# Kernel tuning notes

Hardware: AMD Instinct MI355X
Metric: run time of the kernel (lower is better)

The kernel has to match this reference:

```python
import jax, jax.numpy as jnp
import numpy as np

D, H, K = 384, 6, 8

def _ln(x, g, b, eps=1e-5):
    mu = jnp.mean(x, axis=-1, keepdims=True)
    var = jnp.mean((x - mu) ** 2, axis=-1, keepdims=True)
    return (x - mu) * jax.lax.rsqrt(var + eps) * g + b

def setup_inputs() -> dict:
    key = jax.random.key(0)
    ks = jax.random.split(key, 20)
    B, N = 4, 2048
    s = 0.02
    inp = {
        'x': jax.random.normal(ks[0], (B, N, D), jnp.float32),
        'knn_index': jax.random.randint(ks[1], (B * K * N,), 0, B * N, jnp.int64),
        'ln1_g': jnp.ones((D,), jnp.float32),
        'ln1_b': jnp.zeros((D,), jnp.float32),
        'w_qkv': jax.random.normal(ks[2], (D, 3 * D), jnp.float32) * s,
        'w_proj': jax.random.normal(ks[3], (D, D), jnp.float32) * s,
        'b_proj': jnp.zeros((D,), jnp.float32),
        'w_knn': jax.random.normal(ks[4], (2 * D, D), jnp.float32) * s,
        'b_knn': jnp.zeros((D,), jnp.float32),
        'w_g1': jax.random.normal(ks[5], (2 * D, D), jnp.float32) * s,
        'b_g1': jnp.zeros((D,), jnp.float32),
        'w_g2': jax.random.normal(ks[6], (D, D), jnp.float32) * s,
        'b_g2': jnp.zeros((D,), jnp.float32),
        'ln2_g': jnp.ones((D,), jnp.float32),
        'ln2_b': jnp.zeros((D,), jnp.float32),
        'w_fc1': jax.random.normal(ks[7], (D, 4 * D), jnp.float32) * s,
        'b_fc1': jnp.zeros((4 * D,), jnp.float32),
        'w_fc2': jax.random.normal(ks[8], (4 * D, D), jnp.float32) * s,
        'b_fc2': jnp.zeros((D,), jnp.float32),
    }
    return inp

def reference(x, knn_index, ln1_g, ln1_b, w_qkv, w_proj, b_proj, w_knn, b_knn,
              w_g1, b_g1, w_g2, b_g2, ln2_g, ln2_b, w_fc1, b_fc1, w_fc2, b_fc2):
    B, N, _ = x.shape
    hd = D // H
    scale = hd ** -0.5
    nx = _ln(x, ln1_g, ln1_b)
    # --- self attention ---
    qkv = (nx @ w_qkv).reshape(B, N, 3, H, hd).transpose(2, 0, 3, 1, 4)  # [3,B,H,N,hd]
    q, k, v = qkv[0], qkv[1], qkv[2]
    attn = jax.nn.softmax(jnp.einsum('bhnd,bhmd->bhnm', q * scale, k), axis=-1)
    attn_out = jnp.einsum('bhnm,bhmd->bhnd', attn, v).transpose(0, 2, 1, 3).reshape(B, N, D)
    attn_out = attn_out @ w_proj + b_proj
    # --- EdgeConv-style graph feature: gather-concat-MLP-maxpool ---
    feat = nx.reshape(B * N, D)[knn_index].reshape(B, K, N, D)
    xe = jnp.broadcast_to(nx[:, None], (B, K, N, D))
    gf = jnp.concatenate([feat - xe, xe], axis=-1)  # [B,K,N,2D]
    knn_out = jnp.max(jax.nn.leaky_relu(gf @ w_knn + b_knn, 0.2), axis=1)  # [B,N,D]
    # --- salience gate ---
    gi = jnp.concatenate([attn_out, knn_out], axis=-1)
    gate = jax.nn.sigmoid(jax.nn.gelu(gi @ w_g1 + b_g1, approximate=False) @ w_g2 + b_g2)
    fused = (1 - gate) * attn_out + gate * knn_out
    x = x + fused
    # --- FFN ---
    h = jax.nn.gelu(_ln(x, ln2_g, ln2_b) @ w_fc1 + b_fc1, approximate=False)
    x = x + (h @ w_fc2 + b_fc2)
    return x
```

## Files before the change

kernel.cpp:

```cpp
#include <hip/hip_runtime.h>
#include <math.h>

typedef unsigned short u16;
typedef __attribute__((ext_vector_type(8))) short short8;
typedef __attribute__((ext_vector_type(4))) float floatx4;
typedef __attribute__((ext_vector_type(4))) short sh4v;

union sh4u { sh4v v; u16 u[4]; };
union sh8u { short8 v; u16 u[8]; };

__device__ __forceinline__ floatx4 mfma16(short8 a, short8 b, floatx4 c) {
  return __builtin_amdgcn_mfma_f32_16x16x32_bf16(a, b, c, 0, 0, 0);
}

__device__ __forceinline__ floatx4 zero4() {
  floatx4 z = {0.f, 0.f, 0.f, 0.f};
  return z;
}

__device__ __forceinline__ u16 f2b(float f) {
  union { float f; unsigned u; } v; v.f = f;
  unsigned u = v.u;
  return (u16)((u + 0x7FFFu + ((u >> 16) & 1u)) >> 16);
}

__device__ __forceinline__ float b2f(u16 u) {
  union { unsigned u; float f; } v; v.u = ((unsigned)u) << 16;
  return v.f;
}

__device__ __forceinline__ float gelu_exact(float x) {
  return 0.5f * x * (1.f + erff(x * 0.70710678118654752440f));
}

__device__ __forceinline__ unsigned pack2(float a, float b) {
  return (unsigned)f2b(a) | ((unsigned)f2b(b) << 16);
}

__device__ __forceinline__ unsigned permpack(float p0, float p1) {
  return __builtin_amdgcn_perm(__float_as_uint(p1), __float_as_uint(p0), 0x07060302u);
}

__global__ __launch_bounds__(256) void tcln_kernel(
    const float* __restrict__ p0, const float* __restrict__ p1,
    const float* __restrict__ p2, const float* __restrict__ p3,
    const float* __restrict__ p4, const float* __restrict__ p5,
    const float* __restrict__ wknn,
    u16* __restrict__ o0, u16* __restrict__ o1, u16* __restrict__ o2,
    u16* __restrict__ o3, u16* __restrict__ o4, u16* __restrict__ o5,
    u16* __restrict__ wcT,
    const float* __restrict__ x, const float* __restrict__ g,
    const float* __restrict__ bia, u16* __restrict__ nx) {
  __shared__ u16 L[64][66];
  int t = blockIdx.x, tid = threadIdx.x;
  if (t >= 612) {
    int wave = tid >> 6, lane = tid & 63;
    int row = (t - 612) * 4 + wave;
    const float* xr = x + (size_t)row * 384;
    float v[6];
    float s = 0.f;
#pragma unroll
    for (int j = 0; j < 6; j++) { v[j] = xr[lane + 64 * j]; s += v[j]; }
#pragma unroll
    for (int off = 32; off > 0; off >>= 1) s += __shfl_xor(s, off);
    float mu = s * (1.f / 384.f);
    float ss = 0.f;
#pragma unroll
    for (int j = 0; j < 6; j++) { float d = v[j] - mu; ss += d * d; }
#pragma unroll
    for (int off = 32; off > 0; off >>= 1) ss += __shfl_xor(ss, off);
    float rstd = rsqrtf(ss * (1.f / 384.f) + 1e-5f);
    u16* orow = nx + (size_t)row * 384;
#pragma unroll
    for (int j = 0; j < 6; j++) {
      int d = lane + 64 * j;
      orow[d] = f2b((v[j] - mu) * rstd * g[d] + bia[d]);
    }
    return;
  }
  if (t >= 540) {
    t -= 540;
    int tk = t / 12, tn = t % 12;
    int k0 = tk * 64, j0 = tn * 64;
#pragma unroll
    for (int i = 0; i < 4; i++) {
      int c = tid + 256 * i;
      int r = c >> 4, c4 = (c & 15) * 4;
      floatx4 v;
      if (j0 < 384) {
        v = *(const floatx4*)(wknn + (size_t)(k0 + r) * 384 + j0 + c4);
      } else {
        floatx4 a = *(const floatx4*)(wknn + (size_t)(384 + k0 + r) * 384 + (j0 - 384) + c4);
        floatx4 b = *(const floatx4*)(wknn + (size_t)(k0 + r) * 384 + (j0 - 384) + c4);
        v = a - b;
      }
      *(unsigned*)&L[r][c4]     = pack2(v[0], v[1]);
      *(unsigned*)&L[r][c4 + 2] = pack2(v[2], v[3]);
    }
    __syncthreads();
#pragma unroll
    for (int i = 0; i < 2; i++) {
      int c = tid + 256 * i;
      int nn = c >> 3, k8 = (c & 7) * 8;
      sh8u pk;
#pragma unroll
      for (int j = 0; j < 8; j++) pk.u[j] = L[k8 + j][nn];
      *(short8*)(wcT + (size_t)(j0 + nn) * 384 + k0 + k8) = pk.v;
    }
    return;
  }
  const float* src; u16* dst; int Kd, Nd, tk, tn;
  if      (t < 108) { src = p0; dst = o0; Kd = 384;  Nd = 1152; tk = t / 18; tn = t % 18; }
  else if (t < 144) { src = p1; dst = o1; Kd = 384;  Nd = 384;  t -= 108; tk = t / 6;  tn = t % 6; }
  else if (t < 216) { src = p2; dst = o2; Kd = 768;  Nd = 384;  t -= 144; tk = t / 6;  tn = t % 6; }
  else if (t < 252) { src = p3; dst = o3; Kd = 384;  Nd = 384;  t -= 216; tk = t / 6;  tn = t % 6; }
  else if (t < 396) { src = p4; dst = o4; Kd = 384;  Nd = 1536; t -= 252; tk = t / 24; tn = t % 24; }
  else              { src = p5; dst = o5; Kd = 1536; Nd = 384;  t -= 396; tk = t / 6;  tn = t % 6; }
  int k0 = tk * 64, n0 = tn * 64;
#pragma unroll
  for (int i = 0; i < 4; i++) {
    int c = tid + 256 * i;
    int r = c >> 4, c4 = (c & 15) * 4;
    floatx4 v = *(const floatx4*)(src + (size_t)(k0 + r) * Nd + n0 + c4);
    *(unsigned*)&L[r][c4]     = pack2(v[0], v[1]);
    *(unsigned*)&L[r][c4 + 2] = pack2(v[2], v[3]);
  }
  __syncthreads();
#pragma unroll
  for (int i = 0; i < 2; i++) {
    int c = tid + 256 * i;
    int nn = c >> 3, k8 = (c & 7) * 8;
    sh8u pk;
#pragma unroll
    for (int j = 0; j < 8; j++) pk.u[j] = L[k8 + j][nn];
    *(short8*)(dst + (size_t)(n0 + nn) * Kd + k0 + k8) = pk.v;
  }
}

__global__ __launch_bounds__(256) void lnb_kernel(const u16* __restrict__ x,
                                                  const float* __restrict__ g,
                                                  const float* __restrict__ bia,
                                                  u16* __restrict__ out) {
  int wave = threadIdx.x >> 6, lane = threadIdx.x & 63;
  int row = blockIdx.x * 4 + wave;
  const u16* xr = x + (size_t)row * 384;
  float v[6];
  float s = 0.f;
#pragma unroll
  for (int j = 0; j < 6; j++) { v[j] = b2f(xr[lane + 64 * j]); s += v[j]; }
#pragma unroll
  for (int off = 32; off > 0; off >>= 1) s += __shfl_xor(s, off);
  float mu = s * (1.f / 384.f);
  float ss = 0.f;
#pragma unroll
  for (int j = 0; j < 6; j++) { float d = v[j] - mu; ss += d * d; }
#pragma unroll
  for (int off = 32; off > 0; off >>= 1) ss += __shfl_xor(ss, off);
  float rstd = rsqrtf(ss * (1.f / 384.f) + 1e-5f);
  u16* orow = out + (size_t)row * 384;
#pragma unroll
  for (int j = 0; j < 6; j++) {
    int d = lane + 64 * j;
    orow[d] = f2b((v[j] - mu) * rstd * g[d] + bia[d]);
  }
}

template <int EPI>
__global__ __launch_bounds__(256) void gemm128_kernel(
    const u16* __restrict__ A0, const u16* __restrict__ BwT,
    const u16* __restrict__ BwT2, int N, int K,
    const float* __restrict__ bias, u16* __restrict__ outB, u16* __restrict__ outB2,
    u16* __restrict__ outV) {
  __shared__ u16 As[128][72];
  __shared__ u16 Bs[128][72];
  int tid = threadIdx.x;
  int lane = tid & 63, wave = tid >> 6, quad = lane >> 4, l16 = lane & 15;
  int n0 = blockIdx.x * 128, m0 = blockIdx.y * 128;
  int wm = (wave >> 1) * 64, wn = (wave & 1) * 64;
  const u16* Bsrc = BwT;
  int nbase = n0;
  if (EPI == 8 && n0 >= 1152) { Bsrc = BwT2; nbase = n0 - 1152; }
  floatx4 acc[4][4];
#pragma unroll
  for (int i = 0; i < 4; i++)
#pragma unroll
    for (int j = 0; j < 4; j++) acc[i][j] = zero4();

  for (int k0 = 0; k0 < K; k0 += 64) {
#pragma unroll
    for (int i = 0; i < 4; i++) {
      int c = tid + 256 * i;
      int row = c >> 3, c8 = (c & 7) * 8;
      *(short8*)&As[row][c8] =
          *(const short8*)(A0 + (size_t)(m0 + row) * K + k0 + c8);
      *(short8*)&Bs[row][c8] =
          *(const short8*)(Bsrc + (size_t)(nbase + row) * K + k0 + c8);
    }
    __syncthreads();
#pragma unroll
    for (int kh = 0; kh < 2; kh++) {
      short8 af[4], bfr[4];
#pragma unroll
      for (int ti = 0; ti < 4; ti++)
        af[ti] = *(const short8*)&As[wm + ti * 16 + l16][kh * 32 + quad * 8];
#pragma unroll
      for (int tj = 0; tj < 4; tj++)
        bfr[tj] = *(const short8*)&Bs[wn + tj * 16 + l16][kh * 32 + quad * 8];
#pragma unroll
      for (int ti = 0; ti < 4; ti++)
#pragma unroll
        for (int tj = 0; tj < 4; tj++)
          acc[ti][tj] = mfma16(af[ti], bfr[tj], acc[ti][tj]);
    }
    __syncthreads();
  }

#pragma unroll
  for (int ti = 0; ti < 4; ti++)
#pragma unroll
    for (int tj = 0; tj < 4; tj++) {
      int col = n0 + wn + tj * 16 + l16;
      int row0 = m0 + wm + ti * 16 + quad * 4;
      if (EPI == 8) {
        if (n0 < 1152) {
          float sc = (col < 384) ? 0.18033688011112042f : 1.f;
          sh4u pk;
#pragma unroll
          for (int r = 0; r < 4; r++) {
            u16 bv = f2b(acc[ti][tj][r] * sc);
            outB[(size_t)(row0 + r) * 1152 + col] = bv;
            pk.u[r] = bv;
          }
          if (col >= 768) {
            int b = row0 >> 11, n = row0 & 2047;
            int hd = col - 768;
            *(sh4v*)(outV + ((size_t)(b * 6 + (hd >> 6)) * 64 + (hd & 63)) * 2048 + n) = pk.v;
          }
        } else {
#pragma unroll
          for (int r = 0; r < 4; r++)
            outB2[(size_t)(row0 + r) * 768 + (col - 1152)] = f2b(acc[ti][tj][r]);
        }
      } else {
#pragma unroll
        for (int r = 0; r < 4; r++)
          outB[(size_t)(row0 + r) * N + col] = f2b(gelu_exact(acc[ti][tj][r] + bias[col]));
      }
    }
}

template <int EPI>
__global__ __launch_bounds__(256) void gemm64_kernel(
    const u16* __restrict__ A0, const u16* __restrict__ A1, int Ksplit,
    const u16* __restrict__ BwT, int N, int K,
    const float* __restrict__ bias,
    float* __restrict__ outF, u16* __restrict__ outB,
    const u16* __restrict__ eA16, const u16* __restrict__ eK16,
    const float* __restrict__ eX) {
  __shared__ u16 As[64][72];
  __shared__ u16 Bs[128][72];
  int tid = threadIdx.x;
  int lane = tid & 63, w = tid >> 6, quad = lane >> 4, l16 = lane & 15;
  int n0 = blockIdx.x * 128, m0 = blockIdx.y * 64;
  int ra = tid >> 3, ca = (tid & 7) * 8;
  floatx4 acc[4][2];
#pragma unroll
  for (int i = 0; i < 4; i++)
#pragma unroll
    for (int j = 0; j < 2; j++) acc[i][j] = zero4();

  short8 pa[2], pb[4];
  auto loadAB = [&](int k0) {
    const u16* Ap;
    int kk, sA;
    if (k0 < Ksplit) { Ap = A0; kk = k0; sA = Ksplit; }
    else             { Ap = A1; kk = k0 - Ksplit; sA = K - Ksplit; }
    pa[0] = *(const short8*)(Ap + (size_t)(m0 + ra) * sA + kk + ca);
    pa[1] = *(const short8*)(Ap + (size_t)(m0 + ra + 32) * sA + kk + ca);
#pragma unroll
    for (int i = 0; i < 4; i++)
      pb[i] = *(const short8*)(BwT + (size_t)(n0 + ra + 32 * i) * K + k0 + ca);
  };
  loadAB(0);
  int iters = K >> 6;
  for (int kt = 0; kt < iters; kt++) {
    __syncthreads();
    *(short8*)&As[ra][ca] = pa[0];
    *(short8*)&As[ra + 32][ca] = pa[1];
#pragma unroll
    for (int i = 0; i < 4; i++) *(short8*)&Bs[ra + 32 * i][ca] = pb[i];
    __syncthreads();
    if (kt + 1 < iters) loadAB((kt + 1) * 64);
#pragma unroll
    for (int kh = 0; kh < 2; kh++) {
      short8 af[4], bfr[2];
#pragma unroll
      for (int mt = 0; mt < 4; mt++)
        af[mt] = *(const short8*)&As[mt * 16 + l16][kh * 32 + quad * 8];
#pragma unroll
      for (int nt = 0; nt < 2; nt++)
        bfr[nt] = *(const short8*)&Bs[w * 32 + nt * 16 + l16][kh * 32 + quad * 8];
#pragma unroll
      for (int mt = 0; mt < 4; mt++)
#pragma unroll
        for (int nt = 0; nt < 2; nt++)
          acc[mt][nt] = mfma16(af[mt], bfr[nt], acc[mt][nt]);
    }
  }

#pragma unroll
  for (int mt = 0; mt < 4; mt++)
#pragma unroll
    for (int nt = 0; nt < 2; nt++) {
      int col = n0 + w * 32 + nt * 16 + l16;
      int row0 = m0 + mt * 16 + quad * 4;
#pragma unroll
      for (int r = 0; r < 4; r++) {
        size_t rc = (size_t)(row0 + r) * N + col;
        float v = acc[mt][nt][r];
        if (EPI == 3) {
          outB[rc] = f2b(gelu_exact(v + bias[col]));
        } else if (EPI == 4) {
          float gte = 1.f / (1.f + __expf(-(v + bias[col])));
          float fu = (1.f - gte) * b2f(eA16[rc]) + gte * b2f(eK16[rc]);
          outB[rc] = f2b(eX[rc] + fu);
        } else if (EPI == 7) {
          outF[rc] = v + bias[col] + b2f(eA16[rc]);
        }
      }
    }
}

__global__ __launch_bounds__(256) void attn1_kernel(const u16* __restrict__ qkv,
                                                    const u16* __restrict__ Vt,
                                                    u16* __restrict__ OPb,
                                                    float* __restrict__ LS) {
  __shared__ u16 Ks[64][72];
  __shared__ u16 Vts[64][72];
  __shared__ u16 Ps[4][32][72];
  int tid = threadIdx.x;
  int lane = tid & 63, w = tid >> 6, quad = lane >> 4, l16 = lane & 15;
  int bh = blockIdx.y, b = bh / 6, h = bh % 6;
  int q0 = blockIdx.x * 128, split = blockIdx.z;
  const u16* qbase = qkv + (size_t)b * 2048 * 1152 + h * 64;
  const u16* kbase = qbase + 384 + (size_t)split * 512 * 1152;
  const u16* vtb = Vt + (size_t)bh * 64 * 2048 + split * 512;
  short8 qf[2][2];
#pragma unroll
  for (int s = 0; s < 2; s++) {
    int qrow = q0 + w * 32 + s * 16 + l16;
    qf[s][0] = *(const short8*)(qbase + (size_t)qrow * 1152 + quad * 8);
    qf[s][1] = *(const short8*)(qbase + (size_t)qrow * 1152 + 32 + quad * 8);
  }
  short8 ones;
#pragma unroll
  for (int j = 0; j < 8; j++) ones[j] = (short)0x3F80;
  floatx4 O[4][2];
  floatx4 accL[2] = {zero4(), zero4()};
#pragma unroll
  for (int i = 0; i < 4; i++)
#pragma unroll
    for (int s = 0; s < 2; s++) O[i][s] = zero4();

  int rb = tid >> 3, c8 = (tid & 7) * 8;
  short8 rk[2], rv[2];
  rk[0] = *(const short8*)(kbase + (size_t)rb * 1152 + c8);
  rk[1] = *(const short8*)(kbase + (size_t)(rb + 32) * 1152 + c8);
  rv[0] = *(const short8*)(vtb + (size_t)rb * 2048 + c8);
  rv[1] = *(const short8*)(vtb + (size_t)(rb + 32) * 2048 + c8);

  for (int kt = 0; kt < 8; kt++) {
    __syncthreads();
    *(short8*)&Ks[rb][c8] = rk[0];
    *(short8*)&Ks[rb + 32][c8] = rk[1];
    *(short8*)&Vts[rb][c8] = rv[0];
    *(short8*)&Vts[rb + 32][c8] = rv[1];
    __syncthreads();
    if (kt < 7) {
      int key0 = (kt + 1) * 64;
      rk[0] = *(const short8*)(kbase + (size_t)(key0 + rb) * 1152 + c8);
      rk[1] = *(const short8*)(kbase + (size_t)(key0 + rb + 32) * 1152 + c8);
      rv[0] = *(const short8*)(vtb + (size_t)rb * 2048 + key0 + c8);
      rv[1] = *(const short8*)(vtb + (size_t)(rb + 32) * 2048 + key0 + c8);
    }
#pragma unroll
    for (int mt = 0; mt < 4; mt++) {
      short8 k0 = *(const short8*)&Ks[mt * 16 + l16][quad * 8];
      short8 k1 = *(const short8*)&Ks[mt * 16 + l16][32 + quad * 8];
#pragma unroll
      for (int s = 0; s < 2; s++) {
        floatx4 st = mfma16(k0, qf[s][0], zero4());
        st = mfma16(k1, qf[s][1], st);
        uint2 pk;
        pk.x = permpack(exp2f(st[0]), exp2f(st[1]));
        pk.y = permpack(exp2f(st[2]), exp2f(st[3]));
        *(uint2*)&Ps[w][s * 16 + l16][mt * 16 + quad * 4] = pk;
      }
    }
    short8 pf[2][2];
#pragma unroll
    for (int s = 0; s < 2; s++) {
      pf[s][0] = *(const short8*)&Ps[w][s * 16 + l16][quad * 8];
      pf[s][1] = *(const short8*)&Ps[w][s * 16 + l16][32 + quad * 8];
      accL[s] = mfma16(ones, pf[s][0], accL[s]);
      accL[s] = mfma16(ones, pf[s][1], accL[s]);
    }
#pragma unroll
    for (int mt2 = 0; mt2 < 4; mt2++) {
      short8 v0 = *(const short8*)&Vts[mt2 * 16 + l16][quad * 8];
      short8 v1 = *(const short8*)&Vts[mt2 * 16 + l16][32 + quad * 8];
#pragma unroll
      for (int s = 0; s < 2; s++) {
        O[mt2][s] = mfma16(v0, pf[s][0], O[mt2][s]);
        O[mt2][s] = mfma16(v1, pf[s][1], O[mt2][s]);
      }
    }
  }
#pragma unroll
  for (int s = 0; s < 2; s++) {
    int row = b * 2048 + q0 + w * 32 + s * 16 + l16;
    u16* orow = OPb + (size_t)split * 8192 * 384 + (size_t)row * 384 + h * 64;
#pragma unroll
    for (int mt2 = 0; mt2 < 4; mt2++) {
      sh4u pk;
#pragma unroll
      for (int r = 0; r < 4; r++) pk.u[r] = f2b(O[mt2][s][r]);
      *(sh4v*)(orow + mt2 * 16 + quad * 4) = pk.v;
    }
    if (quad == 0) LS[split * 8192 + row] = accL[s][0];
  }
}

__global__ __launch_bounds__(256) void projknn_kernel(
    const u16* __restrict__ OPb, const float* __restrict__ LS,
    const u16* __restrict__ BwT, const float* __restrict__ bias,
    u16* __restrict__ outB,
    const u16* __restrict__ GBb, const int* __restrict__ kidx,
    const float* __restrict__ bknn, u16* __restrict__ knn_bf) {
  __shared__ u16 As[128][72];
  __shared__ u16 Bs[128][72];
  int bid = blockIdx.x, tid = threadIdx.x;
  if (bid >= 192) {
    int wave = tid >> 6, lane = tid & 63;
    int row = (bid - 192) * 4 + wave;
    int b = row >> 11, n = row & 2047;
    float base[6], acc[6];
#pragma unroll
    for (int j = 0; j < 6; j++) {
      int d = lane + 64 * j;
      base[j] = b2f(GBb[(size_t)row * 768 + 384 + d]) + bknn[d];
      acc[j] = -1e30f;
    }
    for (int kk = 0; kk < 8; kk++) {
      int g = kidx[(b * 8 + kk) * 2048 + n];
      const u16* Gr = GBb + (size_t)g * 768;
#pragma unroll
      for (int j = 0; j < 6; j++) {
        float v = b2f(Gr[lane + 64 * j]) + base[j];
        v = v > 0.f ? v : 0.2f * v;
        acc[j] = fmaxf(acc[j], v);
      }
    }
#pragma unroll
    for (int j = 0; j < 6; j++)
      knn_bf[(size_t)row * 384 + lane + 64 * j] = f2b(acc[j]);
    return;
  }
  int lane = tid & 63, wave = tid >> 6, quad = lane >> 4, l16 = lane & 15;
  int n0 = (bid % 3) * 128, m0 = (bid / 3) * 128;
  int wm = (wave >> 1) * 64, wn = (wave & 1) * 64;
  floatx4 acc[4][4];
#pragma unroll
  for (int i = 0; i < 4; i++)
#pragma unroll
    for (int j = 0; j < 4; j++) acc[i][j] = zero4();

  const size_t SP = (size_t)8192 * 384;
  for (int k0 = 0; k0 < 384; k0 += 64) {
#pragma unroll
    for (int i = 0; i < 4; i++) {
      int c = tid + 256 * i;
      int row = c >> 3, c8 = (c & 7) * 8;
      int gr = m0 + row;
      float rl = 1.f / ((LS[gr] + LS[8192 + gr]) + (LS[16384 + gr] + LS[24576 + gr]));
      const u16* p0 = OPb + (size_t)gr * 384 + k0 + c8;
      sh8u a0, a1, a2, a3, pk;
      a0.v = *(const short8*)p0;
      a1.v = *(const short8*)(p0 + SP);
      a2.v = *(const short8*)(p0 + 2 * SP);
      a3.v = *(const short8*)(p0 + 3 * SP);
#pragma unroll
      for (int j = 0; j < 8; j++)
        pk.u[j] = f2b(((b2f(a0.u[j]) + b2f(a1.u[j])) + (b2f(a2.u[j]) + b2f(a3.u[j]))) * rl);
      *(short8*)&As[row][c8] = pk.v;
      *(short8*)&Bs[row][c8] =
          *(const short8*)(BwT + (size_t)(n0 + row) * 384 + k0 + c8);
    }
    __syncthreads();
#pragma unroll
    for (int kh = 0; kh < 2; kh++) {
      short8 af[4], bfr[4];
#pragma unroll
      for (int ti = 0; ti < 4; ti++)
        af[ti] = *(const short8*)&As[wm + ti * 16 + l16][kh * 32 + quad * 8];
#pragma unroll
      for (int tj = 0; tj < 4; tj++)
        bfr[tj] = *(const short8*)&Bs[wn + tj * 16 + l16][kh * 32 + quad * 8];
#pragma unroll
      for (int ti = 0; ti < 4; ti++)
#pragma unroll
        for (int tj = 0; tj < 4; tj++)
          acc[ti][tj] = mfma16(af[ti], bfr[tj], acc[ti][tj]);
    }
    __syncthreads();
  }
#pragma unroll
  for (int ti = 0; ti < 4; ti++)
#pragma unroll
    for (int tj = 0; tj < 4; tj++) {
      int col = n0 + wn + tj * 16 + l16;
      int row0 = m0 + wm + ti * 16 + quad * 4;
#pragma unroll
      for (int r = 0; r < 4; r++)
        outB[(size_t)(row0 + r) * 384 + col] = f2b(acc[ti][tj][r] + bias[col]);
    }
}

extern "C" void kernel_launch(void* const* d_in, const int* in_sizes, int n_in,
                              void* d_out, int out_size, void* d_ws, size_t ws_size,
                              hipStream_t stream) {
  const float* x    = (const float*)d_in[0];
  const int* kidx   = (const int*)d_in[1];
  const float* ln1g = (const float*)d_in[2];
  const float* ln1b = (const float*)d_in[3];
  const float* wqkv = (const float*)d_in[4];
  const float* wproj= (const float*)d_in[5];
  const float* bproj= (const float*)d_in[6];
  const float* wknn = (const float*)d_in[7];
  const float* bknn = (const float*)d_in[8];
  const float* wg1  = (const float*)d_in[9];
  const float* bg1  = (const float*)d_in[10];
  const float* wg2  = (const float*)d_in[11];
  const float* bg2  = (const float*)d_in[12];
  const float* ln2g = (const float*)d_in[13];
  const float* ln2b = (const float*)d_in[14];
  const float* wfc1 = (const float*)d_in[15];
  const float* bfc1 = (const float*)d_in[16];
  const float* wfc2 = (const float*)d_in[17];
  const float* bfc2 = (const float*)d_in[18];
  float* out = (float*)d_out;

  const int M = 8192;
  char* ws = (char*)d_ws;
  size_t off = 0;
  auto alloc = [&](size_t bytes) -> char* {
    char* p = ws + off;
    off += (bytes + 255) & ~(size_t)255;
    return p;
  };
  u16* nx_bf    = (u16*)alloc((size_t)M * 384 * 2);
  u16* qkv_bf   = (u16*)alloc((size_t)M * 1152 * 2);
  u16* attn_bf  = (u16*)alloc((size_t)M * 384 * 2);
  u16* GBb      = (u16*)alloc((size_t)M * 768 * 2);
  u16* knn_bf   = (u16*)alloc((size_t)M * 384 * 2);
  u16* x2b      = (u16*)alloc((size_t)M * 384 * 2);
  u16* t1_bf    = (u16*)alloc((size_t)M * 384 * 2);
  u16* nx2_bf   = (u16*)alloc((size_t)M * 384 * 2);
  u16* Vt_b     = (u16*)alloc((size_t)24 * 64 * 2048 * 2);
  u16* OPb      = (u16*)alloc((size_t)4 * M * 384 * 2);
  float* LS     = (float*)alloc((size_t)4 * M * 4);
  u16* wqkvT    = (u16*)alloc((size_t)1152 * 384 * 2);
  u16* wprojT   = (u16*)alloc(384 * 384 * 2);
  u16* wcT      = (u16*)alloc((size_t)768 * 384 * 2);
  u16* wg1T     = (u16*)alloc((size_t)384 * 768 * 2);
  u16* wg2T     = (u16*)alloc(384 * 384 * 2);
  u16* wfc1T    = (u16*)alloc((size_t)1536 * 384 * 2);
  u16* wfc2T    = (u16*)alloc((size_t)384 * 1536 * 2);
  u16* h_bf     = qkv_bf;

  tcln_kernel<<<2660, 256, 0, stream>>>(wqkv, wproj, wg1, wg2, wfc1, wfc2, wknn,
                                        wqkvT, wprojT, wg1T, wg2T, wfc1T, wfc2T, wcT,
                                        x, ln1g, ln1b, nx_bf);
  gemm128_kernel<8><<<dim3(15, 64), 256, 0, stream>>>(nx_bf, wqkvT, wcT, 1920, 384,
                                                      nullptr, qkv_bf, GBb, Vt_b);
  attn1_kernel<<<dim3(16, 24, 4), 256, 0, stream>>>(qkv_bf, Vt_b, OPb, LS);
  projknn_kernel<<<2240, 256, 0, stream>>>(OPb, LS, wprojT, bproj, attn_bf,
                                           GBb, kidx, bknn, knn_bf);
  gemm64_kernel<3><<<dim3(3, 128), 256, 0, stream>>>(attn_bf, knn_bf, 384, wg1T, 384, 768,
                                                     bg1, nullptr, t1_bf,
                                                     nullptr, nullptr, nullptr);
  gemm64_kernel<4><<<dim3(3, 128), 256, 0, stream>>>(t1_bf, t1_bf, 384, wg2T, 384, 384,
                                                     bg2, nullptr, x2b,
                                                     attn_bf, knn_bf, x);
  lnb_kernel<<<2048, 256, 0, stream>>>(x2b, ln2g, ln2b, nx2_bf);
  gemm128_kernel<3><<<dim3(12, 64), 256, 0, stream>>>(nx2_bf, wfc1T, nullptr, 1536, 384,
                                                      bfc1, h_bf, nullptr, nullptr);
  gemm64_kernel<7><<<dim3(3, 128), 256, 0, stream>>>(h_bf, h_bf, 1536, wfc2T, 384, 1536,
                                                     bfc2, out, nullptr,
                                                     x2b, nullptr, nullptr);
  (void)in_sizes; (void)n_in; (void)out_size; (void)ws_size;
}
```

Measured before the change: 297.8 us.

## Unify GEMMs on 64-row prefetching tile; move knn maxpool into attention launch

```diff
diff --git a/kernel.cpp b/kernel.cpp
--- a/kernel.cpp
+++ b/kernel.cpp
@@ -166,68 +166,80 @@
 }
 
 template <int EPI>
-__global__ __launch_bounds__(256) void gemm128_kernel(
-    const u16* __restrict__ A0, const u16* __restrict__ BwT,
-    const u16* __restrict__ BwT2, int N, int K,
-    const float* __restrict__ bias, u16* __restrict__ outB, u16* __restrict__ outB2,
-    u16* __restrict__ outV) {
-  __shared__ u16 As[128][72];
+__global__ __launch_bounds__(256) void gemm64_kernel(
+    const u16* __restrict__ A0, const u16* __restrict__ A1, int Ksplit,
+    const u16* __restrict__ BwT, const u16* __restrict__ BwT2, int N, int K,
+    const float* __restrict__ bias,
+    float* __restrict__ outF, u16* __restrict__ outB, u16* __restrict__ outB2,
+    const u16* __restrict__ eA16, const u16* __restrict__ eK16,
+    const float* __restrict__ eX, u16* __restrict__ outV) {
+  __shared__ u16 As[64][72];
   __shared__ u16 Bs[128][72];
   int tid = threadIdx.x;
-  int lane = tid & 63, wave = tid >> 6, quad = lane >> 4, l16 = lane & 15;
-  int n0 = blockIdx.x * 128, m0 = blockIdx.y * 128;
-  int wm = (wave >> 1) * 64, wn = (wave & 1) * 64;
+  int lane = tid & 63, w = tid >> 6, quad = lane >> 4, l16 = lane & 15;
+  int n0 = blockIdx.x * 128, m0 = blockIdx.y * 64;
+  int ra = tid >> 3, ca = (tid & 7) * 8;
   const u16* Bsrc = BwT;
   int nbase = n0;
   if (EPI == 8 && n0 >= 1152) { Bsrc = BwT2; nbase = n0 - 1152; }
-  floatx4 acc[4][4];
+  floatx4 acc[4][2];
 #pragma unroll
   for (int i = 0; i < 4; i++)
 #pragma unroll
-    for (int j = 0; j < 4; j++) acc[i][j] = zero4();
-
-  for (int k0 = 0; k0 < K; k0 += 64) {
-#pragma unroll
-    for (int i = 0; i < 4; i++) {
-      int c = tid + 256 * i;
-      int row = c >> 3, c8 = (c & 7) * 8;
-      *(short8*)&As[row][c8] =
-          *(const short8*)(A0 + (size_t)(m0 + row) * K + k0 + c8);
-      *(short8*)&Bs[row][c8] =
-          *(const short8*)(Bsrc + (size_t)(nbase + row) * K + k0 + c8);
-    }
-    __syncthreads();
+    for (int j = 0; j < 2; j++) acc[i][j] = zero4();
+
+  short8 pa[2], pb[4];
+  auto loadAB = [&](int k0) {
+    const u16* Ap;
+    int kk, sA;
+    if (k0 < Ksplit) { Ap = A0; kk = k0; sA = Ksplit; }
+    else             { Ap = A1; kk = k0 - Ksplit; sA = K - Ksplit; }
+    pa[0] = *(const short8*)(Ap + (size_t)(m0 + ra) * sA + kk + ca);
+    pa[1] = *(const short8*)(Ap + (size_t)(m0 + ra + 32) * sA + kk + ca);
+#pragma unroll
+    for (int i = 0; i < 4; i++)
+      pb[i] = *(const short8*)(Bsrc + (size_t)(nbase + ra + 32 * i) * K + k0 + ca);
+  };
+  loadAB(0);
+  int iters = K >> 6;
+  for (int kt = 0; kt < iters; kt++) {
+    __syncthreads();
+    *(short8*)&As[ra][ca] = pa[0];
+    *(short8*)&As[ra + 32][ca] = pa[1];
+#pragma unroll
+    for (int i = 0; i < 4; i++) *(short8*)&Bs[ra + 32 * i][ca] = pb[i];
+    __syncthreads();
+    if (kt + 1 < iters) loadAB((kt + 1) * 64);
 #pragma unroll
     for (int kh = 0; kh < 2; kh++) {
-      short8 af[4], bfr[4];
-#pragma unroll
-      for (int ti = 0; ti < 4; ti++)
-        af[ti] = *(const short8*)&As[wm + ti * 16 + l16][kh * 32 + quad * 8];
-#pragma unroll
-      for (int tj = 0; tj < 4; tj++)
-        bfr[tj] = *(const short8*)&Bs[wn + tj * 16 + l16][kh * 32 + quad * 8];
-#pragma unroll
-      for (int ti = 0; ti < 4; ti++)
-#pragma unroll
-        for (int tj = 0; tj < 4; tj++)
-          acc[ti][tj] = mfma16(af[ti], bfr[tj], acc[ti][tj]);
-    }
-    __syncthreads();
-  }
-
-#pragma unroll
-  for (int ti = 0; ti < 4; ti++)
-#pragma unroll
-    for (int tj = 0; tj < 4; tj++) {
-      int col = n0 + wn + tj * 16 + l16;
-      int row0 = m0 + wm + ti * 16 + quad * 4;
+      short8 af[4], bfr[2];
+#pragma unroll
+      for (int mt = 0; mt < 4; mt++)
+        af[mt] = *(const short8*)&As[mt * 16 + l16][kh * 32 + quad * 8];
+#pragma unroll
+      for (int nt = 0; nt < 2; nt++)
+        bfr[nt] = *(const short8*)&Bs[w * 32 + nt * 16 + l16][kh * 32 + quad * 8];
+#pragma unroll
+      for (int mt = 0; mt < 4; mt++)
+#pragma unroll
+        for (int nt = 0; nt < 2; nt++)
+          acc[mt][nt] = mfma16(af[mt], bfr[nt], acc[mt][nt]);
+    }
+  }
+
+#pragma unroll
+  for (int mt = 0; mt < 4; mt++)
+#pragma unroll
+    for (int nt = 0; nt < 2; nt++) {
+      int col = n0 + w * 32 + nt * 16 + l16;
+      int row0 = m0 + mt * 16 + quad * 4;
       if (EPI == 8) {
-        if (n0 < 1152) {
+        if (col < 1152) {
           float sc = (col < 384) ? 0.18033688011112042f : 1.f;
           sh4u pk;
 #pragma unroll
           for (int r = 0; r < 4; r++) {
-            u16 bv = f2b(acc[ti][tj][r] * sc);
+            u16 bv = f2b(acc[mt][nt][r] * sc);
             outB[(size_t)(row0 + r) * 1152 + col] = bv;
             pk.u[r] = bv;
           }
@@ -239,109 +251,66 @@
         } else {
 #pragma unroll
           for (int r = 0; r < 4; r++)
-            outB2[(size_t)(row0 + r) * 768 + (col - 1152)] = f2b(acc[ti][tj][r]);
+            outB2[(size_t)(row0 + r) * 768 + (col - 1152)] = f2b(acc[mt][nt][r]);
         }
       } else {
 #pragma unroll
-        for (int r = 0; r < 4; r++)
-          outB[(size_t)(row0 + r) * N + col] = f2b(gelu_exact(acc[ti][tj][r] + bias[col]));
-      }
-    }
-}
-
-template <int EPI>
-__global__ __launch_bounds__(256) void gemm64_kernel(
-    const u16* __restrict__ A0, const u16* __restrict__ A1, int Ksplit,
-    const u16* __restrict__ BwT, int N, int K,
-    const float* __restrict__ bias,
-    float* __restrict__ outF, u16* __restrict__ outB,
-    const u16* __restrict__ eA16, const u16* __restrict__ eK16,
-    const float* __restrict__ eX) {
-  __shared__ u16 As[64][72];
-  __shared__ u16 Bs[128][72];
-  int tid = threadIdx.x;
-  int lane = tid & 63, w = tid >> 6, quad = lane >> 4, l16 = lane & 15;
-  int n0 = blockIdx.x * 128, m0 = blockIdx.y * 64;
-  int ra = tid >> 3, ca = (tid & 7) * 8;
-  floatx4 acc[4][2];
-#pragma unroll
-  for (int i = 0; i < 4; i++)
-#pragma unroll
-    for (int j = 0; j < 2; j++) acc[i][j] = zero4();
-
-  short8 pa[2], pb[4];
-  auto loadAB = [&](int k0) {
-    const u16* Ap;
-    int kk, sA;
-    if (k0 < Ksplit) { Ap = A0; kk = k0; sA = Ksplit; }
-    else             { Ap = A1; kk = k0 - Ksplit; sA = K - Ksplit; }
-    pa[0] = *(const short8*)(Ap + (size_t)(m0 + ra) * sA + kk + ca);
-    pa[1] = *(const short8*)(Ap + (size_t)(m0 + ra + 32) * sA + kk + ca);
-#pragma unroll
-    for (int i = 0; i < 4; i++)
-      pb[i] = *(const short8*)(BwT + (size_t)(n0 + ra + 32 * i) * K + k0 + ca);
-  };
-  loadAB(0);
-  int iters = K >> 6;
-  for (int kt = 0; kt < iters; kt++) {
-    __syncthreads();
-    *(short8*)&As[ra][ca] = pa[0];
-    *(short8*)&As[ra + 32][ca] = pa[1];
-#pragma unroll
-    for (int i = 0; i < 4; i++) *(short8*)&Bs[ra + 32 * i][ca] = pb[i];
-    __syncthreads();
-    if (kt + 1 < iters) loadAB((kt + 1) * 64);
-#pragma unroll
-    for (int kh = 0; kh < 2; kh++) {
-      short8 af[4], bfr[2];
-#pragma unroll
-      for (int mt = 0; mt < 4; mt++)
-        af[mt] = *(const short8*)&As[mt * 16 + l16][kh * 32 + quad * 8];
-#pragma unroll
-      for (int nt = 0; nt < 2; nt++)
-        bfr[nt] = *(const short8*)&Bs[w * 32 + nt * 16 + l16][kh * 32 + quad * 8];
-#pragma unroll
-      for (int mt = 0; mt < 4; mt++)
-#pragma unroll
-        for (int nt = 0; nt < 2; nt++)
-          acc[mt][nt] = mfma16(af[mt], bfr[nt], acc[mt][nt]);
-    }
-  }
-
-#pragma unroll
-  for (int mt = 0; mt < 4; mt++)
-#pragma unroll
-    for (int nt = 0; nt < 2; nt++) {
-      int col = n0 + w * 32 + nt * 16 + l16;
-      int row0 = m0 + mt * 16 + quad * 4;
-#pragma unroll
-      for (int r = 0; r < 4; r++) {
-        size_t rc = (size_t)(row0 + r) * N + col;
-        float v = acc[mt][nt][r];
-        if (EPI == 3) {
-          outB[rc] = f2b(gelu_exact(v + bias[col]));
-        } else if (EPI == 4) {
-          float gte = 1.f / (1.f + __expf(-(v + bias[col])));
-          float fu = (1.f - gte) * b2f(eA16[rc]) + gte * b2f(eK16[rc]);
-          outB[rc] = f2b(eX[rc] + fu);
-        } else if (EPI == 7) {
-          outF[rc] = v + bias[col] + b2f(eA16[rc]);
+        for (int r = 0; r < 4; r++) {
+          size_t rc = (size_t)(row0 + r) * N + col;
+          float v = acc[mt][nt][r];
+          if (EPI == 3) {
+            outB[rc] = f2b(gelu_exact(v + bias[col]));
+          } else if (EPI == 4) {
+            float gte = 1.f / (1.f + __expf(-(v + bias[col])));
+            float fu = (1.f - gte) * b2f(eA16[rc]) + gte * b2f(eK16[rc]);
+            outB[rc] = f2b(eX[rc] + fu);
+          } else if (EPI == 7) {
+            outF[rc] = v + bias[col] + b2f(eA16[rc]);
+          }
         }
       }
     }
 }
 
-__global__ __launch_bounds__(256) void attn1_kernel(const u16* __restrict__ qkv,
-                                                    const u16* __restrict__ Vt,
-                                                    u16* __restrict__ OPb,
-                                                    float* __restrict__ LS) {
+__global__ __launch_bounds__(256) void attnknn_kernel(
+    const u16* __restrict__ qkv, const u16* __restrict__ Vt,
+    u16* __restrict__ OPb, float* __restrict__ LS,
+    const u16* __restrict__ GBb, const int* __restrict__ kidx,
+    const float* __restrict__ bknn, u16* __restrict__ knn_bf) {
   __shared__ u16 Ks[64][72];
   __shared__ u16 Vts[64][72];
   __shared__ u16 Ps[4][32][72];
-  int tid = threadIdx.x;
+  int bid = blockIdx.x, tid = threadIdx.x;
   int lane = tid & 63, w = tid >> 6, quad = lane >> 4, l16 = lane & 15;
-  int bh = blockIdx.y, b = bh / 6, h = bh % 6;
-  int q0 = blockIdx.x * 128, split = blockIdx.z;
+  if (bid >= 1536) {
+    int row = (bid - 1536) * 4 + w;
+    int b = row >> 11, n = row & 2047;
+    float base[6], acc[6];
+#pragma unroll
+    for (int j = 0; j < 6; j++) {
+      int d = lane + 64 * j;
+      base[j] = b2f(GBb[(size_t)row * 768 + 384 + d]) + bknn[d];
+      acc[j] = -1e30f;
+    }
+    for (int kk = 0; kk < 8; kk++) {
+      int g = kidx[(b * 8 + kk) * 2048 + n];
+      const u16* Gr = GBb + (size_t)g * 768;
+#pragma unroll
+      for (int j = 0; j < 6; j++) {
+        float v = b2f(Gr[lane + 64 * j]) + base[j];
+        v = v > 0.f ? v : 0.2f * v;
+        acc[j] = fmaxf(acc[j], v);
+      }
+    }
+#pragma unroll
+    for (int j = 0; j < 6; j++)
+      knn_bf[(size_t)row * 384 + lane + 64 * j] = f2b(acc[j]);
+    return;
+  }
+  int split = bid / 384;
+  int rr = bid - split * 384;
+  int bh = rr >> 4, b = bh / 6, h = bh % 6;
+  int q0 = (rr & 15) * 128;
   const u16* qbase = qkv + (size_t)b * 2048 * 1152 + h * 64;
   const u16* kbase = qbase + 384 + (size_t)split * 512 * 1152;
   const u16* vtb = Vt + (size_t)bh * 64 * 2048 + split * 512;
@@ -431,99 +400,84 @@
   }
 }
 
-__global__ __launch_bounds__(256) void projknn_kernel(
+__global__ __launch_bounds__(256) void projc_kernel(
     const u16* __restrict__ OPb, const float* __restrict__ LS,
     const u16* __restrict__ BwT, const float* __restrict__ bias,
-    u16* __restrict__ outB,
-    const u16* __restrict__ GBb, const int* __restrict__ kidx,
-    const float* __restrict__ bknn, u16* __restrict__ knn_bf) {
-  __shared__ u16 As[128][72];
+    u16* __restrict__ outB) {
+  __shared__ u16 As[64][72];
   __shared__ u16 Bs[128][72];
-  int bid = blockIdx.x, tid = threadIdx.x;
-  if (bid >= 192) {
-    int wave = tid >> 6, lane = tid & 63;
-    int row = (bid - 192) * 4 + wave;
-    int b = row >> 11, n = row & 2047;
-    float base[6], acc[6];
-#pragma unroll
-    for (int j = 0; j < 6; j++) {
-      int d = lane + 64 * j;
-      base[j] = b2f(GBb[(size_t)row * 768 + 384 + d]) + bknn[d];
-      acc[j] = -1e30f;
-    }
-    for (int kk = 0; kk < 8; kk++) {
-      int g = kidx[(b * 8 + kk) * 2048 + n];
-      const u16* Gr = GBb + (size_t)g * 768;
-#pragma unroll
-      for (int j = 0; j < 6; j++) {
-        float v = b2f(Gr[lane + 64 * j]) + base[j];
-        v = v > 0.f ? v : 0.2f * v;
-        acc[j] = fmaxf(acc[j], v);
-      }
-    }
-#pragma unroll
-    for (int j = 0; j < 6; j++)
-      knn_bf[(size_t)row * 384 + lane + 64 * j] = f2b(acc[j]);
-    return;
-  }
-  int lane = tid & 63, wave = tid >> 6, quad = lane >> 4, l16 = lane & 15;
-  int n0 = (bid % 3) * 128, m0 = (bid / 3) * 128;
-  int wm = (wave >> 1) * 64, wn = (wave & 1) * 64;
-  floatx4 acc[4][4];
+  int tid = threadIdx.x;
+  int lane = tid & 63, w = tid >> 6, quad = lane >> 4, l16 = lane & 15;
+  int n0 = blockIdx.x * 128, m0 = blockIdx.y * 64;
+  int ra = tid >> 3, ca = (tid & 7) * 8;
+  const size_t SP = (size_t)8192 * 384;
+  floatx4 acc[4][2];
 #pragma unroll
   for (int i = 0; i < 4; i++)
 #pragma unroll
-    for (int j = 0; j < 4; j++) acc[i][j] = zero4();
-
-  const size_t SP = (size_t)8192 * 384;
-  for (int k0 = 0; k0 < 384; k0 += 64) {
-#pragma unroll
-    for (int i = 0; i < 4; i++) {
-      int c = tid + 256 * i;
-      int row = c >> 3, c8 = (c & 7) * 8;
-      int gr = m0 + row;
-      float rl = 1.f / ((LS[gr] + LS[8192 + gr]) + (LS[16384 + gr] + LS[24576 + gr]));
-      const u16* p0 = OPb + (size_t)gr * 384 + k0 + c8;
+    for (int j = 0; j < 2; j++) acc[i][j] = zero4();
+
+  short8 pa[2], pb[4];
+  auto loadAB = [&](int k0) {
+#pragma unroll
+    for (int i = 0; i < 2; i++) {
+      const u16* p = OPb + (size_t)(m0 + ra + 32 * i) * 384 + k0 + ca;
       sh8u a0, a1, a2, a3, pk;
-      a0.v = *(const short8*)p0;
-      a1.v = *(const short8*)(p0 + SP);
-      a2.v = *(const short8*)(p0 + 2 * SP);
-      a3.v = *(const short8*)(p0 + 3 * SP);
+      a0.v = *(const short8*)p;
+      a1.v = *(const short8*)(p + SP);
+      a2.v = *(const short8*)(p + 2 * SP);
+      a3.v = *(const short8*)(p + 3 * SP);
 #pragma unroll
       for (int j = 0; j < 8; j++)
-        pk.u[j] = f2b(((b2f(a0.u[j]) + b2f(a1.u[j])) + (b2f(a2.u[j]) + b2f(a3.u[j]))) * rl);
-      *(short8*)&As[row][c8] = pk.v;
-      *(short8*)&Bs[row][c8] =
-          *(const short8*)(BwT + (size_t)(n0 + row) * 384 + k0 + c8);
-    }
-    __syncthreads();
+        pk.u[j] = f2b((b2f(a0.u[j]) + b2f(a1.u[j])) + (b2f(a2.u[j]) + b2f(a3.u[j])));
+      pa[i] = pk.v;
+    }
+#pragma unroll
+    for (int i = 0; i < 4; i++)
+      pb[i] = *(const short8*)(BwT + (size_t)(n0 + ra + 32 * i) * 384 + k0 + ca);
+  };
+  loadAB(0);
+  for (int kt = 0; kt < 6; kt++) {
+    __syncthreads();
+    *(short8*)&As[ra][ca] = pa[0];
+    *(short8*)&As[ra + 32][ca] = pa[1];
+#pragma unroll
+    for (int i = 0; i < 4; i++) *(short8*)&Bs[ra + 32 * i][ca] = pb[i];
+    __syncthreads();
+    if (kt < 5) loadAB((kt + 1) * 64);
 #pragma unroll
     for (int kh = 0; kh < 2; kh++) {
-      short8 af[4], bfr[4];
-#pragma unroll
-      for (int ti = 0; ti < 4; ti++)
-        af[ti] = *(const short8*)&As[wm + ti * 16 + l16][kh * 32 + quad * 8];
-#pragma unroll
-      for (int tj = 0; tj < 4; tj++)
-        bfr[tj] = *(const short8*)&Bs[wn + tj * 16 + l16][kh * 32 + quad * 8];
-#pragma unroll
-      for (int ti = 0; ti < 4; ti++)
-#pragma unroll
-        for (int tj = 0; tj < 4; tj++)
-          acc[ti][tj] = mfma16(af[ti], bfr[tj], acc[ti][tj]);
-    }
-    __syncthreads();
-  }
-#pragma unroll
-  for (int ti = 0; ti < 4; ti++)
-#pragma unroll
-    for (int tj = 0; tj < 4; tj++) {
-      int col = n0 + wn + tj * 16 + l16;
-      int row0 = m0 + wm + ti * 16 + quad * 4;
+      short8 af[4], bfr[2];
+#pragma unroll
+      for (int mt = 0; mt < 4; mt++)
+        af[mt] = *(const short8*)&As[mt * 16 + l16][kh * 32 + quad * 8];
+#pragma unroll
+      for (int nt = 0; nt < 2; nt++)
+        bfr[nt] = *(const short8*)&Bs[w * 32 + nt * 16 + l16][kh * 32 + quad * 8];
+#pragma unroll
+      for (int mt = 0; mt < 4; mt++)
+#pragma unroll
+        for (int nt = 0; nt < 2; nt++)
+          acc[mt][nt] = mfma16(af[mt], bfr[nt], acc[mt][nt]);
+    }
+  }
+#pragma unroll
+  for (int mt = 0; mt < 4; mt++) {
+    int row0 = m0 + mt * 16 + quad * 4;
+    float rl[4];
+#pragma unroll
+    for (int r = 0; r < 4; r++) {
+      int gr = row0 + r;
+      rl[r] = 1.f / ((LS[gr] + LS[8192 + gr]) + (LS[16384 + gr] + LS[24576 + gr]));
+    }
+#pragma unroll
+    for (int nt = 0; nt < 2; nt++) {
+      int col = n0 + w * 32 + nt * 16 + l16;
 #pragma unroll
       for (int r = 0; r < 4; r++)
-        outB[(size_t)(row0 + r) * 384 + col] = f2b(acc[ti][tj][r] + bias[col]);
-    }
+        outB[(size_t)(row0 + r) * 384 + col] = f2b(acc[mt][nt][r] * rl[r] + bias[col]);
+    }
+  }
 }
 
 extern "C" void kernel_launch(void* const* d_in, const int* in_sizes, int n_in,
@@ -581,22 +535,24 @@
   tcln_kernel<<<2660, 256, 0, stream>>>(wqkv, wproj, wg1, wg2, wfc1, wfc2, wknn,
                                         wqkvT, wprojT, wg1T, wg2T, wfc1T, wfc2T, wcT,
                                         x, ln1g, ln1b, nx_bf);
-  gemm128_kernel<8><<<dim3(15, 64), 256, 0, stream>>>(nx_bf, wqkvT, wcT, 1920, 384,
-                                                      nullptr, qkv_bf, GBb, Vt_b);
-  attn1_kernel<<<dim3(16, 24, 4), 256, 0, stream>>>(qkv_bf, Vt_b, OPb, LS);
-  projknn_kernel<<<2240, 256, 0, stream>>>(OPb, LS, wprojT, bproj, attn_bf,
+  gemm64_kernel<8><<<dim3(15, 128), 256, 0, stream>>>(nx_bf, nx_bf, 384, wqkvT, wcT, 1920, 384,
+                                                      nullptr, nullptr, qkv_bf, GBb,
+                                                      nullptr, nullptr, nullptr, Vt_b);
+  attnknn_kernel<<<3584, 256, 0, stream>>>(qkv_bf, Vt_b, OPb, LS,
                                            GBb, kidx, bknn, knn_bf);
-  gemm64_kernel<3><<<dim3(3, 128), 256, 0, stream>>>(attn_bf, knn_bf, 384, wg1T, 384, 768,
-                                                     bg1, nullptr, t1_bf,
-                                                     nullptr, nullptr, nullptr);
-  gemm64_kernel<4><<<dim3(3, 128), 256, 0, stream>>>(t1_bf, t1_bf, 384, wg2T, 384, 384,
-                                                     bg2, nullptr, x2b,
-                                                     attn_bf, knn_bf, x);
+  projc_kernel<<<dim3(3, 128), 256, 0, stream>>>(OPb, LS, wprojT, bproj, attn_bf);
+  gemm64_kernel<3><<<dim3(3, 128), 256, 0, stream>>>(attn_bf, knn_bf, 384, wg1T, nullptr, 384, 768,
+                                                     bg1, nullptr, t1_bf, nullptr,
+                                                     nullptr, nullptr, nullptr, nullptr);
+  gemm64_kernel<4><<<dim3(3, 128), 256, 0, stream>>>(t1_bf, t1_bf, 384, wg2T, nullptr, 384, 384,
+                                                     bg2, nullptr, x2b, nullptr,
+                                                     attn_bf, knn_bf, x, nullptr);
   lnb_kernel<<<2048, 256, 0, stream>>>(x2b, ln2g, ln2b, nx2_bf);
-  gemm128_kernel<3><<<dim3(12, 64), 256, 0, stream>>>(nx2_bf, wfc1T, nullptr, 1536, 384,
-                                                      bfc1, h_bf, nullptr, nullptr);
-  gemm64_kernel<7><<<dim3(3, 128), 256, 0, stream>>>(h_bf, h_bf, 1536, wfc2T, 384, 1536,
-                                                     bfc2, out, nullptr,
-                                                     x2b, nullptr, nullptr);
+  gemm64_kernel<3><<<dim3(12, 128), 256, 0, stream>>>(nx2_bf, nx2_bf, 384, wfc1T, nullptr, 1536, 384,
+                                                      bfc1, nullptr, h_bf, nullptr,
+                                                      nullptr, nullptr, nullptr, nullptr);
+  gemm64_kernel<7><<<dim3(3, 128), 256, 0, stream>>>(h_bf, h_bf, 1536, wfc2T, nullptr, 384, 1536,
+                                                     bfc2, out, nullptr, nullptr,
+                                                     x2b, nullptr, nullptr, nullptr);
   (void)in_sizes; (void)n_in; (void)out_size; (void)ws_size;
 }
```

After: 278.6 us. 1.07x faster.
